# Optimization experiments

Measured on AMD Instinct MI355X. Metric: run time of the kernel, lower is better.

## Reference

```python
import jax, jax.numpy as jnp
from jax import lax
import numpy as np

BLANK = 0  # blank label index (init_kwargs)


def setup_inputs() -> dict:
    key = jax.random.key(0)
    k1, k2, k3, k4 = jax.random.split(key, 4)
    B, T, U, V1 = 16, 200, 100, 129  # V1 = vocab_size + 1 (incl. blank)
    logits = jax.random.normal(k1, (B, T, U + 1, V1), dtype=jnp.float32)
    # target labels may not be the blank index (0) -> draw from [1, V1)
    labels = jax.random.randint(k2, (B, U), 1, V1, dtype=jnp.int32)
    logit_lens = jax.random.randint(k3, (B,), T // 2, T + 1, dtype=jnp.int32)
    y_lens = jax.random.randint(k4, (B,), U // 2, U + 1, dtype=jnp.int32)
    return {"logits": logits, "labels": labels, "logit_lens": logit_lens, "y_lens": y_lens}


def _rnnt_losses(logits, labels, logit_lens, y_lens):
    """Per-utterance negative log-likelihood of the RNN-T alignment lattice.

    logits: [B, T, U+1, V+1] unnormalized; labels: [B, U] (no blanks).
    """
    B, T, U1, _ = logits.shape
    U = U1 - 1
    lp = jax.nn.log_softmax(logits, axis=-1)            # [B,T,U1,V1]
    blank_lp = lp[..., BLANK]                            # [B,T,U1]
    # label_lp[b,t,u] = lp[b,t,u,labels[b,u]] for u in [0,U)
    label_lp = jnp.take_along_axis(
        lp[:, :, :U, :], labels[:, None, :, None], axis=3
    )[..., 0]                                            # [B,T,U]

    # alpha[t=0, u] = sum_{u'<u} label_lp[0, u']
    row0 = jnp.concatenate(
        [jnp.zeros((B, 1), lp.dtype), jnp.cumsum(label_lp[:, 0, :], axis=1)], axis=1
    )  # [B,U1]

    def t_step(prev_row, xs):
        blank_prev, lab_t = xs                           # [B,U1], [B,U]
        a = prev_row + blank_prev                        # come from (t-1,u) via blank

        def u_step(carry, x):
            a_u, lab_u = x                               # [B], [B]
            new = jnp.logaddexp(a_u, carry + lab_u)      # blank-from-left vs label-from-below
            return new, new

        _, rest = lax.scan(u_step, a[:, 0], (a[:, 1:].T, lab_t.T))  # [U,B]
        row = jnp.concatenate([a[:, :1], rest.T], axis=1)           # [B,U1]
        return row, row

    xs = (jnp.swapaxes(blank_lp[:, :-1, :], 0, 1),       # [T-1,B,U1]
          jnp.swapaxes(label_lp[:, 1:, :], 0, 1))        # [T-1,B,U]
    _, rows = lax.scan(t_step, row0, xs)                 # [T-1,B,U1]
    alpha = jnp.concatenate([row0[None], rows], axis=0)  # [T,B,U1]

    b_idx = jnp.arange(B)
    t_last = logit_lens - 1
    final = alpha[t_last, b_idx, y_lens] + blank_lp[b_idx, t_last, y_lens]
    return -final                                        # [B]


def reference(logits, labels, logit_lens, y_lens):
    losses = _rnnt_losses(logits, labels, logit_lens, y_lens)
    # reduction='mean': divide by target lengths, then mean over batch
    return jnp.mean(losses / y_lens.astype(losses.dtype))
```

## Files before the change

### kernel.cpp

```cpp
#include <hip/hip_runtime.h>
#include <hip/hip_bf16.h>
#include <math.h>

#define BB  16
#define TT  200
#define UU  100
#define UU1 101
#define VV  129
#define NROWS (BB * TT * UU1)
#define ND   301
#define NP   128
#define NEG  (-1.0e30f)

#define BLLA_F2 (BB * ND * NP)
#define BLLA_F4 (BLLA_F2 / 2)

__global__ __launch_bounds__(256) void init_kernel(float4* __restrict__ blla)
{
    int i = blockIdx.x * 256 + threadIdx.x;
    if (i < BLLA_F4) blla[i] = make_float4(NEG, NEG, NEG, NEG);
}

__global__ __launch_bounds__(256) void lse_kernel(
    const float* __restrict__ logits,
    const int*   __restrict__ labels,
    float2* __restrict__ blla)
{
    int g      = threadIdx.x >> 5;
    int lane32 = threadIdx.x & 31;
    int row    = blockIdx.x * 8 + g;
    if (row >= NROWS) return;

    const float* base = logits + (size_t)row * VV;
    float x0 = base[lane32];
    float x1 = base[lane32 + 32];
    float x2 = base[lane32 + 64];
    float x3 = base[lane32 + 96];
    float xt = 0.0f;
    if (lane32 == 0) xt = base[128];

    float s = __expf(x0) + __expf(x1) + __expf(x2) + __expf(x3);
    if (lane32 == 0) s += __expf(xt);
    #pragma unroll
    for (int off = 16; off; off >>= 1) s += __shfl_xor(s, off);
    float lse = __logf(s);

    int u = row % UU1;
    int t = (row / UU1) % TT;
    int b = row / (UU1 * TT);
    int d = t + u + 1;

    float2* rowp = blla + ((size_t)b * ND + d) * NP;

    float labv = 0.0f;
    if (u < UU) {
        int lab = labels[b * UU + u];
        int sl  = lab >> 5;
        float cand = (sl == 0) ? x0 : (sl == 1) ? x1 : (sl == 2) ? x2
                   : (sl == 3) ? x3 : xt;
        labv = __shfl(cand, (lab & 31) | (threadIdx.x & 32));
    }

    if (lane32 == 0) {
        ((float*)(rowp + u))[0] = x0 - lse;
        if (u < UU) ((float*)(rowp + u + 1))[1] = labv - lse;
    }
}

__device__ __forceinline__ float lae(float x, float y) {
    float mx = fmaxf(x, y);
    float dd = fabsf(x - y);
    return mx + __logf(1.0f + __expf(-dd));
}

__global__ __launch_bounds__(64) void dp_kernel(
    const float2* __restrict__ blla,
    const int*   __restrict__ logit_lens,
    const int*   __restrict__ y_lens,
    float* __restrict__ loss_out)
{
    const int b    = blockIdx.x;
    const int lane = threadIdx.x;
    const int u0   = 2 * lane;
    const int u1   = 2 * lane + 1;

    const float4* diag = (const float4*)(blla + (size_t)b * ND * NP);

    const int t_last = logit_lens[b] - 1;
    const int yl     = y_lens[b];
    const int dstar  = t_last + yl;
    const float bf   = ((const float*)(diag + (size_t)(dstar + 1) * 64))[2 * yl];

    float v0 = (lane == 0) ? 0.0f : NEG;
    float v1 = NEG;

    float4 p0 = diag[(size_t)1 * 64 + lane];
    float4 p1 = diag[(size_t)2 * 64 + lane];
    float4 p2 = diag[(size_t)3 * 64 + lane];
    float4 p3 = diag[(size_t)4 * 64 + lane];
    float4 p4 = diag[(size_t)5 * 64 + lane];
    float4 p5 = diag[(size_t)6 * 64 + lane];
    float4 p6 = diag[(size_t)7 * 64 + lane];
    float4 p7 = diag[(size_t)8 * 64 + lane];

    float loss = 0.0f;
    bool  mine = false;

    #pragma unroll 8
    for (int d = 1; d <= 299; ++d) {
        float4 c = p0;
        p0 = p1; p1 = p2; p2 = p3; p3 = p4; p4 = p5; p5 = p6; p6 = p7;
        int dn = d + 8; if (dn > 300) dn = 300;
        p7 = diag[(size_t)dn * 64 + lane];

        float left = __shfl_up(v1, 1);
        if (lane == 0) left = NEG;

        float n0 = lae(v0 + c.x, left + c.y);
        float n1 = lae(v1 + c.z, v0 + c.w);

        if (d == dstar) {
            if (u0 == yl) { loss = -(n0 + bf); mine = true; }
            if (u1 == yl) { loss = -(n1 + bf); mine = true; }
        }
        v0 = n0; v1 = n1;
    }
    if (mine) loss_out[b] = loss;
}

__global__ void finalize_kernel(
    const float* __restrict__ losses,
    const int*   __restrict__ y_lens,
    float* __restrict__ out)
{
    if (threadIdx.x == 0 && blockIdx.x == 0) {
        float s = 0.0f;
        for (int b = 0; b < BB; ++b)
            s += losses[b] / (float)y_lens[b];
        out[0] = s / (float)BB;
    }
}

extern "C" void kernel_launch(void* const* d_in, const int* in_sizes, int n_in,
                              void* d_out, int out_size, void* d_ws, size_t ws_size,
                              hipStream_t stream) {
    const float* logits     = (const float*)d_in[0];
    const int*   labels     = (const int*)d_in[1];
    const int*   logit_lens = (const int*)d_in[2];
    const int*   y_lens     = (const int*)d_in[3];
    float*       out        = (float*)d_out;

    float2* blla    = (float2*)d_ws;
    float*  ws_loss = (float*)((char*)d_ws + (size_t)BLLA_F2 * sizeof(float2));

    init_kernel<<<(BLLA_F4 + 255) / 256, 256, 0, stream>>>((float4*)d_ws);

    lse_kernel<<<(NROWS + 7) / 8, 256, 0, stream>>>(logits, labels, blla);

    dp_kernel<<<BB, 64, 0, stream>>>(blla, logit_lens, y_lens, ws_loss);

    finalize_kernel<<<1, 64, 0, stream>>>(ws_loss, y_lens, out);
}
```

Measured before the change: 285.6 us.

## Skip out-of-range lattice rows, drop init kernel, fuse finalize into DP

```diff
diff --git a/kernel.cpp b/kernel.cpp
--- a/kernel.cpp
+++ b/kernel.cpp
@@ -1,5 +1,4 @@
 #include <hip/hip_runtime.h>
-#include <hip/hip_bf16.h>
 #include <math.h>
 
 #define BB  16
@@ -13,23 +12,27 @@
 #define NEG  (-1.0e30f)
 
 #define BLLA_F2 (BB * ND * NP)
-#define BLLA_F4 (BLLA_F2 / 2)
-
-__global__ __launch_bounds__(256) void init_kernel(float4* __restrict__ blla)
-{
-    int i = blockIdx.x * 256 + threadIdx.x;
-    if (i < BLLA_F4) blla[i] = make_float4(NEG, NEG, NEG, NEG);
-}
 
 __global__ __launch_bounds__(256) void lse_kernel(
     const float* __restrict__ logits,
     const int*   __restrict__ labels,
-    float2* __restrict__ blla)
+    const int*   __restrict__ logit_lens,
+    const int*   __restrict__ y_lens,
+    float2* __restrict__ blla,
+    int*    __restrict__ ctr)
 {
+    if (blockIdx.x == 0 && threadIdx.x == 0) *ctr = 0;
+
     int g      = threadIdx.x >> 5;
     int lane32 = threadIdx.x & 31;
     int row    = blockIdx.x * 8 + g;
     if (row >= NROWS) return;
+
+    int u = row % UU1;
+    int t = (row / UU1) % TT;
+    int b = row / (UU1 * TT);
+
+    if (t >= logit_lens[b] || u > y_lens[b]) return;
 
     const float* base = logits + (size_t)row * VV;
     float x0 = base[lane32];
@@ -45,11 +48,7 @@
     for (int off = 16; off; off >>= 1) s += __shfl_xor(s, off);
     float lse = __logf(s);
 
-    int u = row % UU1;
-    int t = (row / UU1) % TT;
-    int b = row / (UU1 * TT);
     int d = t + u + 1;
-
     float2* rowp = blla + ((size_t)b * ND + d) * NP;
 
     float labv = 0.0f;
@@ -77,12 +76,14 @@
     const float2* __restrict__ blla,
     const int*   __restrict__ logit_lens,
     const int*   __restrict__ y_lens,
-    float* __restrict__ loss_out)
+    float* __restrict__ loss_ws,
+    int*   __restrict__ ctr,
+    float* __restrict__ out)
 {
     const int b    = blockIdx.x;
     const int lane = threadIdx.x;
     const int u0   = 2 * lane;
-    const int u1   = 2 * lane + 1;
+    const int u1   = u0 + 1;
 
     const float4* diag = (const float4*)(blla + (size_t)b * ND * NP);
 
@@ -90,6 +91,11 @@
     const int yl     = y_lens[b];
     const int dstar  = t_last + yl;
     const float bf   = ((const float*)(diag + (size_t)(dstar + 1) * 64))[2 * yl];
+
+    const bool ux0 = (u0 <= UU);
+    const bool uy0 = (u0 >= 1) && (u0 <= UU);
+    const bool ux1 = (u1 <= UU);
+    const bool uy1 = (u1 >= 1) && (u1 <= UU);
 
     float v0 = (lane == 0) ? 0.0f : NEG;
     float v1 = NEG;
@@ -113,11 +119,18 @@
         int dn = d + 8; if (dn > 300) dn = 300;
         p7 = diag[(size_t)dn * 64 + lane];
 
+        int t0 = d - u0;
+        int t1 = t0 - 1;
+        float cx0 = (ux0 && t0 >= 1 && t0 <= TT    ) ? c.x : NEG;
+        float cy0 = (uy0 && t0 >= 0 && t0 <= TT - 1) ? c.y : NEG;
+        float cx1 = (ux1 && t1 >= 1 && t1 <= TT    ) ? c.z : NEG;
+        float cy1 = (uy1 && t1 >= 0 && t1 <= TT - 1) ? c.w : NEG;
+
         float left = __shfl_up(v1, 1);
         if (lane == 0) left = NEG;
 
-        float n0 = lae(v0 + c.x, left + c.y);
-        float n1 = lae(v1 + c.z, v0 + c.w);
+        float n0 = lae(v0 + cx0, left + cy0);
+        float n1 = lae(v1 + cx1, v0 + cy1);
 
         if (d == dstar) {
             if (u0 == yl) { loss = -(n0 + bf); mine = true; }
@@ -125,19 +138,22 @@
         }
         v0 = n0; v1 = n1;
     }
-    if (mine) loss_out[b] = loss;
-}
 
-__global__ void finalize_kernel(
-    const float* __restrict__ losses,
-    const int*   __restrict__ y_lens,
-    float* __restrict__ out)
-{
-    if (threadIdx.x == 0 && blockIdx.x == 0) {
-        float s = 0.0f;
-        for (int b = 0; b < BB; ++b)
-            s += losses[b] / (float)y_lens[b];
-        out[0] = s / (float)BB;
+    if (mine) {
+        __hip_atomic_store(&loss_ws[b], loss, __ATOMIC_RELEASE,
+                           __HIP_MEMORY_SCOPE_AGENT);
+        int old = __hip_atomic_fetch_add(ctr, 1, __ATOMIC_ACQ_REL,
+                                         __HIP_MEMORY_SCOPE_AGENT);
+        if (old == BB - 1) {
+            __threadfence();
+            float s = 0.0f;
+            for (int i = 0; i < BB; ++i) {
+                float li = __hip_atomic_load(&loss_ws[i], __ATOMIC_RELAXED,
+                                             __HIP_MEMORY_SCOPE_AGENT);
+                s += li / (float)y_lens[i];
+            }
+            out[0] = s / (float)BB;
+        }
     }
 }
 
@@ -152,12 +168,11 @@
 
     float2* blla    = (float2*)d_ws;
     float*  ws_loss = (float*)((char*)d_ws + (size_t)BLLA_F2 * sizeof(float2));
+    int*    ws_ctr  = (int*)(ws_loss + BB);
 
-    init_kernel<<<(BLLA_F4 + 255) / 256, 256, 0, stream>>>((float4*)d_ws);
+    lse_kernel<<<(NROWS + 7) / 8, 256, 0, stream>>>(
+        logits, labels, logit_lens, y_lens, blla, ws_ctr);
 
-    lse_kernel<<<(NROWS + 7) / 8, 256, 0, stream>>>(logits, labels, blla);
-
-    dp_kernel<<<BB, 64, 0, stream>>>(blla, logit_lens, y_lens, ws_loss);
-
-    finalize_kernel<<<1, 64, 0, stream>>>(ws_loss, y_lens, out);
+    dp_kernel<<<BB, 64, 0, stream>>>(
+        blla, logit_lens, y_lens, ws_loss, ws_ctr, out);
 }
```

Measured after the change: 281.0 us. About the same (-1.6%).
